# Kernel tuning notes

Measured on AMD Instinct MI355X. Metric: run time of the kernel, lower is better.

The kernel has to match this reference:

```python
import jax, jax.numpy as jnp
import numpy as np

B, H, W, C = 32, 112, 112, 192
KH = KW = 3


def setup_inputs() -> dict:
    key = jax.random.key(0)
    k1, k2 = jax.random.split(key)
    x = jax.random.normal(k1, (B, H, W, C), dtype=jnp.float32)
    # depthwise kernel, HWIO with I=1 and feature_group_count=C (depth_multiplier=1)
    w = jax.random.normal(k2, (KH, KW, 1, C), dtype=jnp.float32) * 0.1
    b = jnp.zeros((C,), dtype=jnp.float32)
    return {"x": x, "w": w, "b": b}


def reference(x, w, b):
    # Depthwise conv = grouped conv with feature_group_count == channels_in.
    # stride 1, 'same' padding, dilation 1, depth_multiplier 1, linear activation.
    out = jax.lax.conv_general_dilated(
        x, w,
        window_strides=(1, 1),
        padding='SAME',
        rhs_dilation=(1, 1),
        dimension_numbers=('NHWC', 'HWIO', 'NHWC'),
        feature_group_count=C,
    )
    return out + b  # bias broadcast over channel axis
```

## Files before the change

kernel.cpp:

```cpp
#include <hip/hip_runtime.h>
#include <cstdint>


constexpr int Bn = 32, Hn = 112, Wn = 112, Cn = 192, C4 = 48;
constexpr int HT = 4, WT = 16, CT = 16;
constexpr int HTiles = Hn / HT;
constexpr int WTiles = Wn / WT;
constexpr int CTiles = C4 / CT;
constexpr int LR = HT + 2;
constexpr int LW = WT + 2;
constexpr int NF4 = LR * LW * CT;
constexpr int NCHUNK = NF4 / 64;

typedef float floatx4 __attribute__((ext_vector_type(4)));

__device__ __forceinline__ floatx4 fma4(floatx4 a, floatx4 b, floatx4 c) {
  c.x = fmaf(a.x, b.x, c.x);
  c.y = fmaf(a.y, b.y, c.y);
  c.z = fmaf(a.z, b.z, c.z);
  c.w = fmaf(a.w, b.w, c.w);
  return c;
}

__global__ __launch_bounds__(256, 4) void dwconv3x3_lds(
    const float* __restrict__ x,
    const float* __restrict__ wgt,
    const float* __restrict__ bias,
    float* __restrict__ out) {
  __shared__ floatx4 lds[NF4];
  int tid = (int)threadIdx.x;
  int lane = tid & 63;
  int wave = tid >> 6;

  int bid = blockIdx.x;
  int chunk = gridDim.x >> 3;
  int sbid = (bid & 7) * chunk + (bid >> 3);
  int c4t = sbid % CTiles; int t = sbid / CTiles;
  int wt = t % WTiles;     t /= WTiles;
  int ht = t % HTiles;     int b = t / HTiles;

  int h0 = ht * HT, w0 = wt * WT;
  int cbase = c4t * (CT * 4);
  const float* xb = x + (long)b * Hn * Wn * Cn + cbase;

  for (int k = wave; k < NCHUNK; k += 4) {
    int linear = k * 64 + lane;
    int c4i = linear & 15;
    int t2 = linear >> 4;
    int wi = t2 % LW;
    int ri = t2 / LW;
    int h = h0 + ri - 1;
    int wg = w0 + wi - 1;
    int hc = min(max(h, 0), Hn - 1);
    int wc = min(max(wg, 0), Wn - 1);
    const float* src = xb + ((long)hc * Wn + wc) * Cn + c4i * 4;
    __builtin_amdgcn_global_load_lds(
        (const __attribute__((address_space(1))) void*)src,
        (__attribute__((address_space(3))) void*)&lds[k * 64], 16, 0, 0);
  }

  int c4i = tid & 15;
  int wi1 = tid >> 4;
  int cofs = cbase + c4i * 4;
  floatx4 wv[3][3];
#pragma unroll
  for (int kh = 0; kh < 3; ++kh)
#pragma unroll
    for (int kw = 0; kw < 3; ++kw)
      wv[kh][kw] = *(const floatx4*)(wgt + (kh * 3 + kw) * Cn + cofs);
  floatx4 bv = *(const floatx4*)(bias + cofs);
  floatx4 acc[HT];
#pragma unroll
  for (int o = 0; o < HT; ++o) acc[o] = bv;

  int wg1 = w0 + wi1;
  float cs0 = (wg1 - 1 >= 0) ? 1.f : 0.f;
  float cs2 = (wg1 + 1 < Wn) ? 1.f : 0.f;

  asm volatile("s_waitcnt vmcnt(0)" ::: "memory");
  __syncthreads();

#pragma unroll
  for (int r = 0; r < LR; ++r) {
    int h = h0 + r - 1;
    float s1 = (h >= 0 && h < Hn) ? 1.f : 0.f;
    const floatx4* base = &lds[(r * LW + wi1) * CT + c4i];
    floatx4 xv0 = base[0] * (s1 * cs0);
    floatx4 xv1 = base[CT] * s1;
    floatx4 xv2 = base[2 * CT] * (s1 * cs2);
#pragma unroll
    for (int kh = 0; kh < 3; ++kh) {
      int o = r - kh;
      if (o >= 0 && o < HT) {
        acc[o] = fma4(xv0, wv[kh][0], acc[o]);
        acc[o] = fma4(xv1, wv[kh][1], acc[o]);
        acc[o] = fma4(xv2, wv[kh][2], acc[o]);
      }
    }
  }

  long of4 = (((long)b * Hn + h0) * Wn + wg1) * C4 + c4t * CT + c4i;
  floatx4* op = (floatx4*)out + of4;
  const int ostride = Wn * C4;
#pragma unroll
  for (int o = 0; o < HT; ++o)
    __builtin_nontemporal_store(acc[o], op + (long)o * ostride);
}

extern "C" void kernel_launch(void* const* d_in, const int* in_sizes, int n_in,
                              void* d_out, int out_size, void* d_ws, size_t ws_size,
                              hipStream_t stream) {
  const float* x = (const float*)d_in[0];
  const float* w = (const float*)d_in[1];
  const float* b = (const float*)d_in[2];
  float* out = (float*)d_out;

  const int grid = Bn * HTiles * WTiles * CTiles;
  dwconv3x3_lds<<<grid, 256, 0, stream>>>(x, w, b, out);
}
```

Measured before the change: 119.9 us.

## Stream rows through an LDS ring buffer with persistent row-group blocks

Each block now walks 28 output rows in 7 steps, staging input rows into a 10-slot LDS ring via async global-to-LDS loads. The loads for upcoming rows are issued before computing the current step, with partial vmcnt waits and barriers. This reuses the halo rows between consecutive steps instead of reloading them per 4-row tile, and overlaps loads with compute. Column boundary masks are folded into the weights. The trade-off is far fewer blocks (grid 2688), lower occupancy (launch bounds 3), and two barriers per step.

```diff
diff --git a/kernel.cpp b/kernel.cpp
--- a/kernel.cpp
+++ b/kernel.cpp
@@ -1,16 +1,15 @@
 #include <hip/hip_runtime.h>
-#include <cstdint>
 
 
 constexpr int Bn = 32, Hn = 112, Wn = 112, Cn = 192, C4 = 48;
 constexpr int HT = 4, WT = 16, CT = 16;
-constexpr int HTiles = Hn / HT;
-constexpr int WTiles = Wn / WT;
-constexpr int CTiles = C4 / CT;
-constexpr int LR = HT + 2;
-constexpr int LW = WT + 2;
-constexpr int NF4 = LR * LW * CT;
-constexpr int NCHUNK = NF4 / 64;
+constexpr int NSTEP = 7;
+constexpr int HG = 4;
+constexpr int WTiles = 7, CTiles = 3;
+constexpr int LW = 20;
+constexpr int ROWF4 = LW * CT;
+constexpr int ROWB = ROWF4 * 16;
+constexpr int RING = 10;
 
 typedef float floatx4 __attribute__((ext_vector_type(4)));
 
@@ -22,89 +21,119 @@
   return c;
 }
 
-__global__ __launch_bounds__(256, 4) void dwconv3x3_lds(
+__global__ __launch_bounds__(256, 3) void dwconv3x3_stream(
     const float* __restrict__ x,
     const float* __restrict__ wgt,
     const float* __restrict__ bias,
     float* __restrict__ out) {
-  __shared__ floatx4 lds[NF4];
-  int tid = (int)threadIdx.x;
-  int lane = tid & 63;
-  int wave = tid >> 6;
+  __shared__ floatx4 lds[RING * ROWF4];
+  const int tid = (int)threadIdx.x;
+  const int lane = tid & 63;
+  const int wave = tid >> 6;
 
   int bid = blockIdx.x;
   int chunk = gridDim.x >> 3;
   int sbid = (bid & 7) * chunk + (bid >> 3);
-  int c4t = sbid % CTiles; int t = sbid / CTiles;
-  int wt = t % WTiles;     t /= WTiles;
-  int ht = t % HTiles;     int b = t / HTiles;
+  int c4t = sbid % CTiles; int t0 = sbid / CTiles;
+  int wt = t0 % WTiles;    t0 /= WTiles;
+  int hg = t0 % HG;        int b = t0 / HG;
 
-  int h0 = ht * HT, w0 = wt * WT;
-  int cbase = c4t * (CT * 4);
-  const float* xb = x + (long)b * Hn * Wn * Cn + cbase;
+  const int hbase = hg * (HT * NSTEP);
+  const int w0 = wt * WT;
+  const int cbase = c4t * (CT * 4);
+  const float* xb = x + (long)b * Hn * Wn * Cn;
 
-  for (int k = wave; k < NCHUNK; k += 4) {
-    int linear = k * 64 + lane;
-    int c4i = linear & 15;
-    int t2 = linear >> 4;
-    int wi = t2 % LW;
-    int ri = t2 / LW;
-    int h = h0 + ri - 1;
-    int wg = w0 + wi - 1;
-    int hc = min(max(h, 0), Hn - 1);
-    int wc = min(max(wg, 0), Wn - 1);
-    const float* src = xb + ((long)hc * Wn + wc) * Cn + c4i * 4;
-    __builtin_amdgcn_global_load_lds(
-        (const __attribute__((address_space(1))) void*)src,
-        (__attribute__((address_space(3))) void*)&lds[k * 64], 16, 0, 0);
+  int colOff[5];
+  {
+    int c4l = lane & 15;
+#pragma unroll
+    for (int j = 0; j < 5; ++j) {
+      int wi = j * 4 + (lane >> 4);
+      int wg = w0 + wi - 1;
+      int wc = min(max(wg, 0), Wn - 1);
+      colOff[j] = wc * Cn + cbase + c4l * 4;
+    }
   }
 
-  int c4i = tid & 15;
-  int wi1 = tid >> 4;
-  int cofs = cbase + c4i * 4;
+  auto stageRow = [&](int row) {
+    int h = hbase + row - 1;
+    int hc = min(max(h, 0), Hn - 1);
+    const float* rowp = xb + (long)hc * (Wn * Cn);
+    int slot = row % RING;
+    char* ldsbase = (char*)lds + slot * ROWB;
+#pragma unroll
+    for (int j = 0; j < 5; ++j) {
+      __builtin_amdgcn_global_load_lds(
+          (const __attribute__((address_space(1))) void*)(rowp + colOff[j]),
+          (__attribute__((address_space(3))) void*)(ldsbase + j * 1024),
+          16, 0, 0);
+    }
+  };
+
+  stageRow(wave);
+  stageRow(4 + (wave & 1));
+
+  const int c4i = tid & 15;
+  const int wi1 = tid >> 4;
+  const int cofs = cbase + c4i * 4;
+  const int wg1 = w0 + wi1;
+  const float cs0 = (wg1 >= 1) ? 1.f : 0.f;
+  const float cs2 = (wg1 <= Wn - 2) ? 1.f : 0.f;
   floatx4 wv[3][3];
 #pragma unroll
-  for (int kh = 0; kh < 3; ++kh)
+  for (int kh = 0; kh < 3; ++kh) {
 #pragma unroll
     for (int kw = 0; kw < 3; ++kw)
       wv[kh][kw] = *(const floatx4*)(wgt + (kh * 3 + kw) * Cn + cofs);
-  floatx4 bv = *(const floatx4*)(bias + cofs);
-  floatx4 acc[HT];
-#pragma unroll
-  for (int o = 0; o < HT; ++o) acc[o] = bv;
+    wv[kh][0] *= cs0;
+    wv[kh][2] *= cs2;
+  }
+  const floatx4 bv = *(const floatx4*)(bias + cofs);
 
-  int wg1 = w0 + wi1;
-  float cs0 = (wg1 - 1 >= 0) ? 1.f : 0.f;
-  float cs2 = (wg1 + 1 < Wn) ? 1.f : 0.f;
+  const float sTop = (hg == 0) ? 0.f : 1.f;
+  const float sBot = (hg == HG - 1) ? 0.f : 1.f;
 
-  asm volatile("s_waitcnt vmcnt(0)" ::: "memory");
-  __syncthreads();
+  const int ostrideF4 = Wn * C4;
+  floatx4* outp = (floatx4*)out +
+      ((long)b * Hn + hbase) * ostrideF4 + (long)wg1 * C4 + c4t * CT + c4i;
 
 #pragma unroll
-  for (int r = 0; r < LR; ++r) {
-    int h = h0 + r - 1;
-    float s1 = (h >= 0 && h < Hn) ? 1.f : 0.f;
-    const floatx4* base = &lds[(r * LW + wi1) * CT + c4i];
-    floatx4 xv0 = base[0] * (s1 * cs0);
-    floatx4 xv1 = base[CT] * s1;
-    floatx4 xv2 = base[2 * CT] * (s1 * cs2);
+  for (int t = 0; t < NSTEP; ++t) {
+    stageRow(4 * t + 6 + wave);
+    if (t == 0) asm volatile("s_waitcnt vmcnt(5)" ::: "memory");
+    else        asm volatile("s_waitcnt vmcnt(9)" ::: "memory");
+    __builtin_amdgcn_s_barrier();
+
+    floatx4 acc[HT];
 #pragma unroll
-    for (int kh = 0; kh < 3; ++kh) {
-      int o = r - kh;
-      if (o >= 0 && o < HT) {
-        acc[o] = fma4(xv0, wv[kh][0], acc[o]);
-        acc[o] = fma4(xv1, wv[kh][1], acc[o]);
-        acc[o] = fma4(xv2, wv[kh][2], acc[o]);
+    for (int o = 0; o < HT; ++o) acc[o] = bv;
+
+#pragma unroll
+    for (int r = 0; r < 6; ++r) {
+      const int slot = (4 * t + r) % RING;
+      const floatx4* base = lds + slot * ROWF4 + wi1 * 16 + c4i;
+      floatx4 xv0 = base[0];
+      floatx4 xv1 = base[16];
+      floatx4 xv2 = base[32];
+      if (t == 0 && r == 0) { xv0 *= sTop; xv1 *= sTop; xv2 *= sTop; }
+      if (t == NSTEP - 1 && r == 5) { xv0 *= sBot; xv1 *= sBot; xv2 *= sBot; }
+#pragma unroll
+      for (int kh = 0; kh < 3; ++kh) {
+        int o = r - kh;
+        if (o >= 0 && o < HT) {
+          acc[o] = fma4(xv0, wv[kh][0], acc[o]);
+          acc[o] = fma4(xv1, wv[kh][1], acc[o]);
+          acc[o] = fma4(xv2, wv[kh][2], acc[o]);
+        }
       }
     }
+
+#pragma unroll
+    for (int o = 0; o < HT; ++o)
+      __builtin_nontemporal_store(acc[o], outp + (long)(4 * t + o) * ostrideF4);
+
+    __builtin_amdgcn_s_barrier();
   }
-
-  long of4 = (((long)b * Hn + h0) * Wn + wg1) * C4 + c4t * CT + c4i;
-  floatx4* op = (floatx4*)out + of4;
-  const int ostride = Wn * C4;
-#pragma unroll
-  for (int o = 0; o < HT; ++o)
-    __builtin_nontemporal_store(acc[o], op + (long)o * ostride);
 }
 
 extern "C" void kernel_launch(void* const* d_in, const int* in_sizes, int n_in,
@@ -115,6 +144,6 @@
   const float* b = (const float*)d_in[2];
   float* out = (float*)d_out;
 
-  const int grid = Bn * HTiles * WTiles * CTiles;
-  dwconv3x3_lds<<<grid, 256, 0, stream>>>(x, w, b, out);
+  const int grid = Bn * HG * WTiles * CTiles;
+  dwconv3x3_stream<<<grid, 256, 0, stream>>>(x, w, b, out);
 }
```

Result: faster. 106.9 us (-10.8%).
